# Kernel optimization log

Measured on AMD Instinct MI355X. Metric: run time of the kernel, lower is better.

## Reference

```python
import jax, jax.numpy as jnp
import numpy as np

B, S, V, H = 64, 512, 128, 1024
TEMP = 1.0


def _lstm_layer(x_seq, W_ih, W_hh, b_ih, b_hh):
    """x_seq: (S, B, D_in) -> (S, B, H). PyTorch gate order: i, f, g, o."""
    Hh = W_hh.shape[1]
    Bb = x_seq.shape[1]
    # precompute input projections for all timesteps: (S, B, 4H)
    xW = jnp.einsum('sbd,gd->sbg', x_seq, W_ih) + (b_ih + b_hh)

    def step(carry, xw_t):
        h, c = carry
        gates = xw_t + h @ W_hh.T  # (B, 4H)
        i, f, g, o = jnp.split(gates, 4, axis=-1)
        i = jax.nn.sigmoid(i)
        f = jax.nn.sigmoid(f)
        g = jnp.tanh(g)
        o = jax.nn.sigmoid(o)
        c = f * c + i * g
        h = o * jnp.tanh(c)
        return (h, c), h

    h0 = jnp.zeros((Bb, Hh), dtype=x_seq.dtype)
    c0 = jnp.zeros((Bb, Hh), dtype=x_seq.dtype)
    _, hs = jax.lax.scan(step, (h0, c0), xW)
    return hs  # (S, B, H)


def setup_inputs() -> dict:
    key = jax.random.key(0)
    ks = jax.random.split(key, 11)
    s = 1.0 / np.sqrt(H)
    u = lambda k, shape: jax.random.uniform(k, shape, jnp.float32, -s, s)
    return {
        'x': jax.random.normal(ks[0], (B, S, V), jnp.float32),
        'W_ih0': u(ks[1], (4 * H, V)),
        'W_hh0': u(ks[2], (4 * H, H)),
        'b_ih0': u(ks[3], (4 * H,)),
        'b_hh0': u(ks[4], (4 * H,)),
        'W_ih1': u(ks[5], (4 * H, H)),
        'W_hh1': u(ks[6], (4 * H, H)),
        'b_ih1': u(ks[7], (4 * H,)),
        'b_hh1': u(ks[8], (4 * H,)),
        'W_fc': u(ks[9], (V, H)),
        'b_fc': u(ks[10], (V,)),
    }


def reference(x, W_ih0, W_hh0, b_ih0, b_hh0, W_ih1, W_hh1, b_ih1, b_hh1, W_fc, b_fc):
    xs = jnp.transpose(x, (1, 0, 2))  # (S, B, V)
    h1 = _lstm_layer(xs, W_ih0, W_hh0, b_ih0, b_hh0)   # (S, B, H)
    h2 = _lstm_layer(h1, W_ih1, W_hh1, b_ih1, b_hh1)   # (S, B, H)
    logits = jnp.einsum('sbh,vh->sbv', h2, W_fc) + b_fc  # (S, B, V)
    out = jax.nn.log_softmax(logits * TEMP, axis=-1)
    return jnp.transpose(out, (1, 0, 2))  # (B, S, V)
```

## Files before the change

kernel.cpp:

```cpp
#include <hip/hip_runtime.h>
#include <hip/hip_bf16.h>
#include <math.h>


#define S_LEN 512
#define B_SZ  64
#define V_SZ  128
#define H_SZ  1024
#define BH    65536
#define RING  64
#define SLOT  66560
#define FSTR  16
#define INVP  48

typedef unsigned short u16;
typedef unsigned short u16x8 __attribute__((ext_vector_type(8)));
typedef __bf16         bf16x8 __attribute__((ext_vector_type(8)));
typedef float          f32x4  __attribute__((ext_vector_type(4)));
typedef int            i32x4  __attribute__((ext_vector_type(4)));

__device__ __forceinline__ u16 f2bf(float f) {
    unsigned int u = __float_as_uint(f);
    u += 0x7fffu + ((u >> 16) & 1u);
    return (u16)(u >> 16);
}
__device__ __forceinline__ f32x4 mfma16(u16x8 a, u16x8 b, f32x4 c) {
    return __builtin_amdgcn_mfma_f32_16x16x32_bf16(
        __builtin_bit_cast(bf16x8, a), __builtin_bit_cast(bf16x8, b), c, 0, 0, 0);
}
__device__ __forceinline__ f32x4 mfma16(i32x4 a, u16x8 b, f32x4 c) {
    return __builtin_amdgcn_mfma_f32_16x16x32_bf16(
        __builtin_bit_cast(bf16x8, a), __builtin_bit_cast(bf16x8, b), c, 0, 0, 0);
}

__device__ __forceinline__ void ld_g(i32x4& d, const u16* p) {
    asm volatile("global_load_dwordx4 %0, %1, off" : "=v"(d) : "v"(p));
}
__device__ __forceinline__ void st_coh_u16(u16* p, u16 v) {
    unsigned int vv = v;
    asm volatile("global_store_short %0, %1, off sc0 sc1" :: "v"(p), "v"(vv));
}
__device__ __forceinline__ int ld_flag(const int* p) {
    int v;
    asm volatile("global_load_dword %0, %1, off sc0 sc1\n\ts_waitcnt vmcnt(0)"
                 : "=v"(v) : "v"(p) : "memory");
    return v;
}
__device__ __forceinline__ void st_flag(int* p, int v) {
    asm volatile("global_store_dword %0, %1, off sc0 sc1" :: "v"(p), "v"(v));
}
#define WAITV(n) asm volatile("s_waitcnt vmcnt(" #n ")" ::: "memory")
#define SCHEDB   __builtin_amdgcn_sched_barrier(0)

__device__ __forceinline__ void l2_acquire_inv() {
    __builtin_amdgcn_fence(__ATOMIC_ACQUIRE, "agent");
}

__global__ __launch_bounds__(256) void cvt_kernel(const float* __restrict__ s,
                                                  u16* __restrict__ d, int n)
{
    int i = (blockIdx.x * 256 + threadIdx.x) * 4;
    if (i >= n) return;
    float4 v = *(const float4*)(s + i);
    ushort4 o;
    o.x = f2bf(v.x); o.y = f2bf(v.y); o.z = f2bf(v.z); o.w = f2bf(v.w);
    *(ushort4*)(d + i) = o;
}

union SMemL {
    struct { u16 wih[4 * 4 * 64 * 8]; u16 whh[32 * 4 * 64 * 8]; } l0;
    struct { u16 w[2 * 32 * 2 * 64 * 8]; } l1;
    float lg[16][132];
};

__global__ __launch_bounds__(256, 1) void persist_kernel(
    const float* __restrict__ x,
    const u16* __restrict__ Wih0c, const u16* __restrict__ Whh0c,
    const u16* __restrict__ Wih1c, const u16* __restrict__ Whh1c,
    const u16* __restrict__ Wfcc,
    const float* __restrict__ bih0, const float* __restrict__ bhh0,
    const float* __restrict__ bih1, const float* __restrict__ bhh1,
    const float* __restrict__ bfc,
    u16* __restrict__ h0b, u16* __restrict__ h1b,
    int* __restrict__ flagL0, int* __restrict__ flagL1, int* __restrict__ flagFC,
    float* __restrict__ out)
{
    __shared__ SMemL sm;
    const int bid = blockIdx.x, tid = threadIdx.x;
    const int wave = tid >> 6, lane = tid & 63;
    const int l16 = lane & 15, kgi = lane >> 4, kg8 = kgi * 8;

    if (bid < 64) {
        const int j0 = bid * 16, jj = j0 + l16;
        #pragma unroll
        for (int i = 0; i < 4; ++i) {
            int f = tid + i * 256;
            int rl = f >> 4, kf = f & 15;
            int c = kf >> 2, kg = kf & 3;
            int g = rl >> 4, jl = rl & 15;
            int gr = g * H_SZ + j0 + jl;
            *(u16x8*)&sm.l0.wih[(((c * 4 + g) * 64) + kg * 16 + jl) * 8] =
                *(const u16x8*)(Wih0c + (size_t)gr * V_SZ + kf * 8);
        }
        #pragma unroll
        for (int i = 0; i < 32; ++i) {
            int f = tid + i * 256;
            int rl = f >> 7, kf = f & 127;
            int c = kf >> 2, kg = kf & 3;
            int g = rl >> 4, jl = rl & 15;
            int gr = g * H_SZ + j0 + jl;
            *(u16x8*)&sm.l0.whh[(((c * 4 + g) * 64) + kg * 16 + jl) * 8] =
                *(const u16x8*)(Whh0c + (size_t)gr * H_SZ + kf * 8);
        }
        __syncthreads();

        const float bii = bih0[jj]            + bhh0[jj];
        const float bif = bih0[H_SZ + jj]     + bhh0[H_SZ + jj];
        const float big = bih0[2 * H_SZ + jj] + bhh0[2 * H_SZ + jj];
        const float bio = bih0[3 * H_SZ + jj] + bhh0[3 * H_SZ + jj];

        const int arow = wave * 16 + l16;
        const float* xrow = x + (size_t)arow * (S_LEN * V_SZ);
        float creg[4] = {0.f, 0.f, 0.f, 0.f};

        for (int t = 0; t < S_LEN; ++t) {
            {
                const int* p = nullptr; int tgt = 0;
                if (tid < 64)                        { p = flagL0 + tid * FSTR;        tgt = t; }
                else if (tid < 192 && t >= RING)     { p = flagL1 + (tid - 64) * FSTR; tgt = t - (RING - 1); }
                if (p && tgt > 0) while (ld_flag(p) < tgt) __builtin_amdgcn_s_sleep(2);
                __syncthreads();
            }
            if (t >= INVP && (t % INVP) == 0) l2_acquire_inv();

            f32x4 acc[4][2] = {};
            {
                const float* xp = xrow + (size_t)t * V_SZ + kg8;
                #pragma unroll
                for (int i = 0; i < 4; ++i) {
                    float4 u = *(const float4*)(xp + i * 32);
                    float4 v = *(const float4*)(xp + i * 32 + 4);
                    u16x8 af;
                    af[0] = f2bf(u.x); af[1] = f2bf(u.y); af[2] = f2bf(u.z); af[3] = f2bf(u.w);
                    af[4] = f2bf(v.x); af[5] = f2bf(v.y); af[6] = f2bf(v.z); af[7] = f2bf(v.w);
                    #pragma unroll
                    for (int g = 0; g < 4; ++g)
                        acc[g][i & 1] = mfma16(af,
                            *(const u16x8*)&sm.l0.wih[((i * 4 + g) * 64 + lane) * 8], acc[g][i & 1]);
                }
            }
            {
                auto ISSUE = [&](i32x4 (&buf)[8], const u16* base) {
                    #pragma unroll
                    for (int q = 0; q < 8; ++q) ld_g(buf[q], base + q * 32);
                };
                auto COMP = [&](i32x4 (&buf)[8], int k0) {
                    #pragma unroll
                    for (int q = 0; q < 8; ++q) {
                        #pragma unroll
                        for (int g = 0; g < 4; ++g)
                            acc[g][q & 1] = mfma16(buf[q],
                                *(const u16x8*)&sm.l0.whh[(((k0 + q) * 4 + g) * 64 + lane) * 8],
                                acc[g][q & 1]);
                    }
                };
                const u16* aB = h0b + (size_t)((t - 1) & (RING - 1)) * SLOT
                              + (size_t)arow * H_SZ + kg8;
                i32x4 b0[8], b1[8];
                WAITV(0);
                ISSUE(b0, aB);
                ISSUE(b1, aB + 256); WAITV(8); SCHEDB; COMP(b0, 0);
                ISSUE(b0, aB + 512); WAITV(8); SCHEDB; COMP(b1, 8);
                ISSUE(b1, aB + 768); WAITV(8); SCHEDB; COMP(b0, 16);
                                     WAITV(0); SCHEDB; COMP(b1, 24);
            }
            {
                u16* hout = h0b + (size_t)(t & (RING - 1)) * SLOT;
                #pragma unroll
                for (int r = 0; r < 4; ++r) {
                    const int m = wave * 16 + kgi * 4 + r;
                    const float ip = acc[0][0][r] + acc[0][1][r] + bii;
                    const float fp = acc[1][0][r] + acc[1][1][r] + bif;
                    const float gp = acc[2][0][r] + acc[2][1][r] + big;
                    const float op = acc[3][0][r] + acc[3][1][r] + bio;
                    const float iv = 1.f / (1.f + expf(-ip));
                    const float fv = 1.f / (1.f + expf(-fp));
                    const float gv = tanhf(gp);
                    const float ov = 1.f / (1.f + expf(-op));
                    const float cv = fv * creg[r] + iv * gv;
                    creg[r] = cv;
                    st_coh_u16(hout + (size_t)m * H_SZ + jj, f2bf(ov * tanhf(cv)));
                }
                WAITV(0);
            }
            __syncthreads();
            if (tid == 0) st_flag(flagL0 + bid * FSTR, t + 1);
        }
        return;
    }

    if (bid < 192) {
        const int lb = bid - 64, j0 = lb * 8, jj2 = j0 + (l16 & 7);
        #pragma unroll
        for (int i = 0; i < 32; ++i) {
            int f = tid + i * 256;
            int region = f >> 12;
            int r2 = f & 4095;
            int rl = r2 >> 7, kf = r2 & 127;
            int c = kf >> 2, kg = kf & 3;
            int nt = rl >> 4, jl = rl & 15;
            int gr = (rl >> 3) * H_SZ + j0 + (rl & 7);
            const u16* src = (region ? Whh1c : Wih1c) + (size_t)gr * H_SZ + kf * 8;
            *(u16x8*)&sm.l1.w[((((region * 32 + c) * 2 + nt) * 64) + kg * 16 + jl) * 8] =
                *(const u16x8*)src;
        }
        __syncthreads();

        const float bii = bih1[jj2]            + bhh1[jj2];
        const float bif = bih1[H_SZ + jj2]     + bhh1[H_SZ + jj2];
        const float big = bih1[2 * H_SZ + jj2] + bhh1[2 * H_SZ + jj2];
        const float bio = bih1[3 * H_SZ + jj2] + bhh1[3 * H_SZ + jj2];
        const bool lo = (l16 < 8);

        const int arow = wave * 16 + l16;
        float creg[4] = {0.f, 0.f, 0.f, 0.f};

        for (int t = 0; t < S_LEN; ++t) {
            {
                const int* p = nullptr; int tgt = 0;
                if (tid < 64)                        { p = flagL0 + tid * FSTR;         tgt = t + 1; }
                else if (tid < 192)                  { p = flagL1 + (tid - 64) * FSTR;  tgt = t; }
                else if (tid < 196 && t >= RING)     { p = flagFC + (tid - 192) * FSTR; tgt = t - (RING - 1); }
                if (p && tgt > 0) while (ld_flag(p) < tgt) __builtin_amdgcn_s_sleep(2);
                __syncthreads();
            }
            if (t >= INVP && (t % INVP) == 0) l2_acquire_inv();

            f32x4 acc[2][2] = {};
            {
                auto ISSUE = [&](i32x4 (&buf)[8], const u16* base) {
                    #pragma unroll
                    for (int q = 0; q < 8; ++q) ld_g(buf[q], base + q * 32);
                };
                auto COMP = [&](i32x4 (&buf)[8], int region, int c0) {
                    #pragma unroll
                    for (int q = 0; q < 8; ++q) {
                        #pragma unroll
                        for (int nt = 0; nt < 2; ++nt)
                            acc[nt][q & 1] = mfma16(buf[q],
                                *(const u16x8*)&sm.l1.w[(((region * 32 + c0 + q) * 2 + nt) * 64 + lane) * 8],
                                acc[nt][q & 1]);
                    }
                };
                const u16* a1 = h0b + (size_t)(t & (RING - 1)) * SLOT
                              + (size_t)arow * H_SZ + kg8;
                const u16* a2 = h1b + (size_t)((t - 1) & (RING - 1)) * SLOT
                              + (size_t)arow * H_SZ + kg8;
                i32x4 b0[8], b1[8];
                WAITV(0);
                ISSUE(b0, a1);
                ISSUE(b1, a1 + 256); WAITV(8); SCHEDB; COMP(b0, 0, 0);
                ISSUE(b0, a1 + 512); WAITV(8); SCHEDB; COMP(b1, 0, 8);
                ISSUE(b1, a1 + 768); WAITV(8); SCHEDB; COMP(b0, 0, 16);
                ISSUE(b0, a2);       WAITV(8); SCHEDB; COMP(b1, 0, 24);
                ISSUE(b1, a2 + 256); WAITV(8); SCHEDB; COMP(b0, 1, 0);
                ISSUE(b0, a2 + 512); WAITV(8); SCHEDB; COMP(b1, 1, 8);
                ISSUE(b1, a2 + 768); WAITV(8); SCHEDB; COMP(b0, 1, 16);
                                     WAITV(0); SCHEDB; COMP(b1, 1, 24);
            }
            {
                u16* hout = h1b + (size_t)(t & (RING - 1)) * SLOT;
                #pragma unroll
                for (int r = 0; r < 4; ++r) {
                    const float s0 = acc[0][0][r] + acc[0][1][r];
                    const float s1 = acc[1][0][r] + acc[1][1][r];
                    const float q0 = __shfl_xor(s0, 8);
                    const float q1 = __shfl_xor(s1, 8);
                    const float ip = (lo ? s0 : q0) + bii;
                    const float fp = (lo ? q0 : s0) + bif;
                    const float gp = (lo ? s1 : q1) + big;
                    const float op = (lo ? q1 : s1) + bio;
                    const float iv = 1.f / (1.f + expf(-ip));
                    const float fv = 1.f / (1.f + expf(-fp));
                    const float gv = tanhf(gp);
                    const float ov = 1.f / (1.f + expf(-op));
                    const float cv = fv * creg[r] + iv * gv;
                    creg[r] = cv;
                    if (lo) {
                        const int m = wave * 16 + kgi * 4 + r;
                        st_coh_u16(hout + (size_t)m * H_SZ + jj2, f2bf(ov * tanhf(cv)));
                    }
                }
                WAITV(0);
            }
            __syncthreads();
            if (tid == 0) st_flag(flagL1 + lb * FSTR, t + 1);
        }
        return;
    }

    {
        const int fb = bid - 192, m0 = fb * 16;
        const u16* wp[2];
        #pragma unroll
        for (int nt = 0; nt < 2; ++nt)
            wp[nt] = Wfcc + (size_t)(wave * 32 + nt * 16 + l16) * H_SZ + kg8;

        for (int t = 0; t < S_LEN; ++t) {
            {
                const int* p = nullptr; int tgt = 0;
                if (tid < 128) { p = flagL1 + tid * FSTR; tgt = t + 1; }
                if (p && tgt > 0) while (ld_flag(p) < tgt) __builtin_amdgcn_s_sleep(2);
                __syncthreads();
            }
            if (t >= INVP && (t % INVP) == 0) l2_acquire_inv();

            const u16* aB = h1b + (size_t)(t & (RING - 1)) * SLOT
                          + (size_t)(m0 + l16) * H_SZ + kg8;
            f32x4 acc[2][2] = {};
            i32x4 buf[8];
            WAITV(0);
            #pragma unroll
            for (int c = 0; c < 4; ++c) {
                #pragma unroll
                for (int q = 0; q < 8; ++q) ld_g(buf[q], aB + c * 256 + q * 32);
                WAITV(0); SCHEDB;
                #pragma unroll
                for (int q = 0; q < 8; ++q) {
                    #pragma unroll
                    for (int nt = 0; nt < 2; ++nt)
                        acc[nt][q & 1] = mfma16(buf[q],
                            *(const u16x8*)(wp[nt] + (c * 8 + q) * 32), acc[nt][q & 1]);
                }
            }
            #pragma unroll
            for (int nt = 0; nt < 2; ++nt)
                #pragma unroll
                for (int r = 0; r < 4; ++r) {
                    const int m = kgi * 4 + r, n = wave * 32 + nt * 16 + l16;
                    sm.lg[m][n] = acc[nt][0][r] + acc[nt][1][r] + bfc[n];
                }
            __syncthreads();
            const int row = tid >> 4, sub = tid & 15;
            float vals[8]; float mx = -1e30f;
            #pragma unroll
            for (int q = 0; q < 8; ++q) { vals[q] = sm.lg[row][sub * 8 + q]; mx = fmaxf(mx, vals[q]); }
            #pragma unroll
            for (int o = 1; o < 16; o <<= 1) mx = fmaxf(mx, __shfl_xor(mx, o));
            float se = 0.f;
            #pragma unroll
            for (int q = 0; q < 8; ++q) se += expf(vals[q] - mx);
            #pragma unroll
            for (int o = 1; o < 16; o <<= 1) se += __shfl_xor(se, o);
            const float ls = mx + logf(se);
            float* op = out + (size_t)(m0 + row) * (S_LEN * V_SZ) + (size_t)t * V_SZ + sub * 8;
            #pragma unroll
            for (int q = 0; q < 8; ++q) op[q] = vals[q] - ls;

            __syncthreads();
            if (tid == 0) st_flag(flagFC + fb * FSTR, t + 1);
        }
    }
}

extern "C" void kernel_launch(void* const* d_in, const int* in_sizes, int n_in,
                              void* d_out, int out_size, void* d_ws, size_t ws_size,
                              hipStream_t stream)
{
    const float* x    = (const float*)d_in[0];
    const float* Wih0 = (const float*)d_in[1];
    const float* Whh0 = (const float*)d_in[2];
    const float* bih0 = (const float*)d_in[3];
    const float* bhh0 = (const float*)d_in[4];
    const float* Wih1 = (const float*)d_in[5];
    const float* Whh1 = (const float*)d_in[6];
    const float* bih1 = (const float*)d_in[7];
    const float* bhh1 = (const float*)d_in[8];
    const float* Wfc  = (const float*)d_in[9];
    const float* bfc  = (const float*)d_in[10];
    float* out = (float*)d_out;

    u16* wih0 = (u16*)d_ws;
    u16* whh0 = wih0 + (size_t)4096 * 128;
    u16* wih1 = whh0 + (size_t)4096 * 1024;
    u16* whh1 = wih1 + (size_t)4096 * 1024;
    u16* wfc  = whh1 + (size_t)4096 * 1024;
    u16* h0b  = wfc  + (size_t)128 * 1024;
    u16* h1b  = h0b + (size_t)RING * SLOT;
    int* flags  = (int*)(h1b + (size_t)RING * SLOT);
    int* flagL0 = flags;
    int* flagL1 = flagL0 + 64 * FSTR;
    int* flagFC = flagL1 + 128 * FSTR;

    auto cvt = [&](const float* s, u16* d, int n) {
        cvt_kernel<<<(n / 4 + 255) / 256, 256, 0, stream>>>(s, d, n);
    };
    cvt(Wih0, wih0, 4096 * 128);
    cvt(Whh0, whh0, 4096 * 1024);
    cvt(Wih1, wih1, 4096 * 1024);
    cvt(Whh1, whh1, 4096 * 1024);
    cvt(Wfc,  wfc,  128 * 1024);
    hipMemsetAsync(h0b + (size_t)(RING - 1) * SLOT, 0, (size_t)BH * sizeof(u16), stream);
    hipMemsetAsync(h1b + (size_t)(RING - 1) * SLOT, 0, (size_t)BH * sizeof(u16), stream);
    hipMemsetAsync(flags, 0, (size_t)196 * FSTR * sizeof(int), stream);

    persist_kernel<<<196, 256, 0, stream>>>(
        x, wih0, whh0, wih1, whh1, wfc,
        bih0, bhh0, bih1, bhh1, bfc,
        h0b, h1b, flagL0, flagL1, flagFC, out);
}
```

Measured before the change: 6.553 ms.

## Swizzle LDS weights, pre-convert x, vectorize h stores, deepen load pipeline

Stores the recurrent and input weights in LDS as row-major with an XOR swizzle instead of the MFMA-fragment layout. Converts x to bf16 in a separate pre-kernel and prefetches it before the flag wait. Each step's h output is staged through a small LDS transpose buffer so it can be written with coherent 16-byte stores instead of scattered 2-byte stores. The global h loads move to a three-buffer pipeline, and the ring depth and L2 invalidate period shrink. The aims are fewer tiny coherent stores per step, more load latency hidden, and less conversion work on the critical path, at the cost of an extra LDS round trip, more registers, and a smaller ring slack between layers.

```diff
diff --git a/kernel.cpp b/kernel.cpp
--- a/kernel.cpp
+++ b/kernel.cpp
@@ -8,10 +8,10 @@
 #define V_SZ  128
 #define H_SZ  1024
 #define BH    65536
-#define RING  64
+#define RING  32
 #define SLOT  66560
 #define FSTR  16
-#define INVP  48
+#define INVP  20
 
 typedef unsigned short u16;
 typedef unsigned short u16x8 __attribute__((ext_vector_type(8)));
@@ -36,9 +36,9 @@
 __device__ __forceinline__ void ld_g(i32x4& d, const u16* p) {
     asm volatile("global_load_dwordx4 %0, %1, off" : "=v"(d) : "v"(p));
 }
-__device__ __forceinline__ void st_coh_u16(u16* p, u16 v) {
-    unsigned int vv = v;
-    asm volatile("global_store_short %0, %1, off sc0 sc1" :: "v"(p), "v"(vv));
+__device__ __forceinline__ void st_coh16(u16* p, u16x8 v) {
+    i32x4 vv = __builtin_bit_cast(i32x4, v);
+    asm volatile("global_store_dwordx4 %0, %1, off sc0 sc1" :: "v"(p), "v"(vv));
 }
 __device__ __forceinline__ int ld_flag(const int* p) {
     int v;
@@ -50,6 +50,7 @@
     asm volatile("global_store_dword %0, %1, off sc0 sc1" :: "v"(p), "v"(v));
 }
 #define WAITV(n) asm volatile("s_waitcnt vmcnt(" #n ")" ::: "memory")
+#define LGKM0    asm volatile("s_waitcnt lgkmcnt(0)" ::: "memory")
 #define SCHEDB   __builtin_amdgcn_sched_barrier(0)
 
 __device__ __forceinline__ void l2_acquire_inv() {
@@ -68,13 +69,13 @@
 }
 
 union SMemL {
-    struct { u16 wih[4 * 4 * 64 * 8]; u16 whh[32 * 4 * 64 * 8]; } l0;
-    struct { u16 w[2 * 32 * 2 * 64 * 8]; } l1;
+    struct { u16 whh[64 * 1024]; u16 wih[64 * 128]; u16 tr[4][384]; } l0;
+    struct { u16 w[64 * 1024]; u16 tr[4][384]; } l1;
     float lg[16][132];
 };
 
 __global__ __launch_bounds__(256, 1) void persist_kernel(
-    const float* __restrict__ x,
+    const u16* __restrict__ xb,
     const u16* __restrict__ Wih0c, const u16* __restrict__ Whh0c,
     const u16* __restrict__ Wih1c, const u16* __restrict__ Whh1c,
     const u16* __restrict__ Wfcc,
@@ -92,25 +93,17 @@
 
     if (bid < 64) {
         const int j0 = bid * 16, jj = j0 + l16;
-        #pragma unroll
-        for (int i = 0; i < 4; ++i) {
-            int f = tid + i * 256;
-            int rl = f >> 4, kf = f & 15;
-            int c = kf >> 2, kg = kf & 3;
-            int g = rl >> 4, jl = rl & 15;
-            int gr = g * H_SZ + j0 + jl;
-            *(u16x8*)&sm.l0.wih[(((c * 4 + g) * 64) + kg * 16 + jl) * 8] =
-                *(const u16x8*)(Wih0c + (size_t)gr * V_SZ + kf * 8);
-        }
-        #pragma unroll
-        for (int i = 0; i < 32; ++i) {
-            int f = tid + i * 256;
-            int rl = f >> 7, kf = f & 127;
-            int c = kf >> 2, kg = kf & 3;
-            int g = rl >> 4, jl = rl & 15;
-            int gr = g * H_SZ + j0 + jl;
-            *(u16x8*)&sm.l0.whh[(((c * 4 + g) * 64) + kg * 16 + jl) * 8] =
-                *(const u16x8*)(Whh0c + (size_t)gr * H_SZ + kf * 8);
+        for (int ch = tid; ch < 1024; ch += 256) {
+            int row = ch >> 4, kc = ch & 15;
+            int gr = (row >> 4) * H_SZ + j0 + (row & 15);
+            int bo = (row * 256 + kc * 16) ^ ((row & 7) << 4);
+            *(u16x8*)((char*)sm.l0.wih + bo) = *(const u16x8*)(Wih0c + (size_t)gr * V_SZ + kc * 8);
+        }
+        for (int ch = tid; ch < 8192; ch += 256) {
+            int row = ch >> 7, kc = ch & 127;
+            int gr = (row >> 4) * H_SZ + j0 + (row & 15);
+            int bo = (row * 2048 + kc * 16) ^ ((row & 7) << 4);
+            *(u16x8*)((char*)sm.l0.whh + bo) = *(const u16x8*)(Whh0c + (size_t)gr * H_SZ + kc * 8);
         }
         __syncthreads();
 
@@ -119,66 +112,70 @@
         const float big = bih0[2 * H_SZ + jj] + bhh0[2 * H_SZ + jj];
         const float bio = bih0[3 * H_SZ + jj] + bhh0[3 * H_SZ + jj];
 
+        const int swz = (l16 & 7) << 4;
+        int whh_rb[4], wih_rb[4];
+        #pragma unroll
+        for (int g = 0; g < 4; ++g) {
+            whh_rb[g] = (g * 16 + l16) * 2048 + kgi * 16;
+            wih_rb[g] = (g * 16 + l16) * 256 + kgi * 16;
+        }
         const int arow = wave * 16 + l16;
-        const float* xrow = x + (size_t)arow * (S_LEN * V_SZ);
+        const u16* xrow = xb + (size_t)arow * (S_LEN * V_SZ);
+        u16* trw = sm.l0.tr[wave];
         float creg[4] = {0.f, 0.f, 0.f, 0.f};
 
         for (int t = 0; t < S_LEN; ++t) {
+            i32x4 xq[4];
+            {
+                const u16* xp = xrow + (size_t)t * V_SZ + kg8;
+                #pragma unroll
+                for (int i = 0; i < 4; ++i) ld_g(xq[i], xp + i * 32);
+            }
             {
                 const int* p = nullptr; int tgt = 0;
-                if (tid < 64)                        { p = flagL0 + tid * FSTR;        tgt = t; }
-                else if (tid < 192 && t >= RING)     { p = flagL1 + (tid - 64) * FSTR; tgt = t - (RING - 1); }
+                if (tid < 64)                      { p = flagL0 + tid * FSTR;        tgt = t; }
+                else if (tid < 192 && t >= RING)   { p = flagL1 + (tid - 64) * FSTR; tgt = t - (RING - 1); }
                 if (p && tgt > 0) while (ld_flag(p) < tgt) __builtin_amdgcn_s_sleep(2);
                 __syncthreads();
             }
             if (t >= INVP && (t % INVP) == 0) l2_acquire_inv();
+            WAITV(0); SCHEDB;
 
             f32x4 acc[4][2] = {};
-            {
-                const float* xp = xrow + (size_t)t * V_SZ + kg8;
-                #pragma unroll
-                for (int i = 0; i < 4; ++i) {
-                    float4 u = *(const float4*)(xp + i * 32);
-                    float4 v = *(const float4*)(xp + i * 32 + 4);
-                    u16x8 af;
-                    af[0] = f2bf(u.x); af[1] = f2bf(u.y); af[2] = f2bf(u.z); af[3] = f2bf(u.w);
-                    af[4] = f2bf(v.x); af[5] = f2bf(v.y); af[6] = f2bf(v.z); af[7] = f2bf(v.w);
+            auto ISSUE = [&](i32x4 (&buf)[8], const u16* base) {
+                #pragma unroll
+                for (int q = 0; q < 8; ++q) ld_g(buf[q], base + q * 32);
+            };
+            auto COMP = [&](i32x4 (&buf)[8], int k0) {
+                #pragma unroll
+                for (int q = 0; q < 8; ++q)
                     #pragma unroll
                     for (int g = 0; g < 4; ++g)
-                        acc[g][i & 1] = mfma16(af,
-                            *(const u16x8*)&sm.l0.wih[((i * 4 + g) * 64 + lane) * 8], acc[g][i & 1]);
-                }
-            }
-            {
-                auto ISSUE = [&](i32x4 (&buf)[8], const u16* base) {
-                    #pragma unroll
-                    for (int q = 0; q < 8; ++q) ld_g(buf[q], base + q * 32);
-                };
-                auto COMP = [&](i32x4 (&buf)[8], int k0) {
-                    #pragma unroll
-                    for (int q = 0; q < 8; ++q) {
-                        #pragma unroll
-                        for (int g = 0; g < 4; ++g)
-                            acc[g][q & 1] = mfma16(buf[q],
-                                *(const u16x8*)&sm.l0.whh[(((k0 + q) * 4 + g) * 64 + lane) * 8],
-                                acc[g][q & 1]);
-                    }
-                };
-                const u16* aB = h0b + (size_t)((t - 1) & (RING - 1)) * SLOT
-                              + (size_t)arow * H_SZ + kg8;
-                i32x4 b0[8], b1[8];
-                WAITV(0);
-                ISSUE(b0, aB);
-                ISSUE(b1, aB + 256); WAITV(8); SCHEDB; COMP(b0, 0);
-                ISSUE(b0, aB + 512); WAITV(8); SCHEDB; COMP(b1, 8);
-                ISSUE(b1, aB + 768); WAITV(8); SCHEDB; COMP(b0, 16);
-                                     WAITV(0); SCHEDB; COMP(b1, 24);
-            }
+                        acc[g][q & 1] = mfma16(buf[q],
+                            *(const u16x8*)((char*)sm.l0.whh + ((whh_rb[g] + (k0 + q) * 64) ^ swz)),
+                            acc[g][q & 1]);
+            };
+            const u16* aB = h0b + (size_t)((t - 1) & (RING - 1)) * SLOT
+                          + (size_t)arow * H_SZ + kg8;
+            i32x4 b0[8], b1[8], b2[8];
+            ISSUE(b0, aB); ISSUE(b1, aB + 256); ISSUE(b2, aB + 512);
+            SCHEDB;
+            #pragma unroll
+            for (int i = 0; i < 4; ++i)
+                #pragma unroll
+                for (int g = 0; g < 4; ++g)
+                    acc[g][i & 1] = mfma16(xq[i],
+                        *(const u16x8*)((char*)sm.l0.wih + ((wih_rb[g] + i * 64) ^ swz)),
+                        acc[g][i & 1]);
+            WAITV(16); SCHEDB; COMP(b0, 0);  ISSUE(b0, aB + 768);
+            WAITV(16); SCHEDB; COMP(b1, 8);
+            WAITV(8);  SCHEDB; COMP(b2, 16);
+            WAITV(0);  SCHEDB; COMP(b0, 24);
+
             {
                 u16* hout = h0b + (size_t)(t & (RING - 1)) * SLOT;
                 #pragma unroll
                 for (int r = 0; r < 4; ++r) {
-                    const int m = wave * 16 + kgi * 4 + r;
                     const float ip = acc[0][0][r] + acc[0][1][r] + bii;
                     const float fp = acc[1][0][r] + acc[1][1][r] + bif;
                     const float gp = acc[2][0][r] + acc[2][1][r] + big;
@@ -189,7 +186,13 @@
                     const float ov = 1.f / (1.f + expf(-op));
                     const float cv = fv * creg[r] + iv * gv;
                     creg[r] = cv;
-                    st_coh_u16(hout + (size_t)m * H_SZ + jj, f2bf(ov * tanhf(cv)));
+                    trw[(kgi * 4 + r) * 24 + l16] = f2bf(ov * tanhf(cv));
+                }
+                LGKM0; SCHEDB;
+                if (lane < 32) {
+                    int m = lane >> 1, jb = lane & 1;
+                    u16x8 v = *(const u16x8*)&trw[m * 24 + jb * 8];
+                    st_coh16(hout + (size_t)(wave * 16 + m) * H_SZ + j0 + jb * 8, v);
                 }
                 WAITV(0);
             }
@@ -201,18 +204,13 @@
 
     if (bid < 192) {
         const int lb = bid - 64, j0 = lb * 8, jj2 = j0 + (l16 & 7);
-        #pragma unroll
-        for (int i = 0; i < 32; ++i) {
-            int f = tid + i * 256;
-            int region = f >> 12;
-            int r2 = f & 4095;
-            int rl = r2 >> 7, kf = r2 & 127;
-            int c = kf >> 2, kg = kf & 3;
-            int nt = rl >> 4, jl = rl & 15;
+        for (int ch = tid; ch < 8192; ch += 256) {
+            int ldsrow = ch >> 7, kc = ch & 127;
+            int region = ldsrow >> 5, rl = ldsrow & 31;
             int gr = (rl >> 3) * H_SZ + j0 + (rl & 7);
-            const u16* src = (region ? Whh1c : Wih1c) + (size_t)gr * H_SZ + kf * 8;
-            *(u16x8*)&sm.l1.w[((((region * 32 + c) * 2 + nt) * 64) + kg * 16 + jl) * 8] =
-                *(const u16x8*)src;
+            const u16* src = (region ? Whh1c : Wih1c) + (size_t)gr * H_SZ + kc * 8;
+            int bo = (ldsrow * 2048 + kc * 16) ^ ((ldsrow & 7) << 4);
+            *(u16x8*)((char*)sm.l1.w + bo) = *(const u16x8*)src;
         }
         __syncthreads();
 
@@ -222,7 +220,15 @@
         const float bio = bih1[3 * H_SZ + jj2] + bhh1[3 * H_SZ + jj2];
         const bool lo = (l16 < 8);
 
+        const int swz = (l16 & 7) << 4;
+        int wrb[2][2];
+        #pragma unroll
+        for (int region = 0; region < 2; ++region)
+            #pragma unroll
+            for (int nt = 0; nt < 2; ++nt)
+                wrb[region][nt] = (region * 32 + nt * 16 + l16) * 2048 + kgi * 16;
         const int arow = wave * 16 + l16;
+        u16* trw = sm.l1.tr[wave];
         float creg[4] = {0.f, 0.f, 0.f, 0.f};
 
         for (int t = 0; t < S_LEN; ++t) {
@@ -237,39 +243,34 @@
             if (t >= INVP && (t % INVP) == 0) l2_acquire_inv();
 
             f32x4 acc[2][2] = {};
-            {
-                auto ISSUE = [&](i32x4 (&buf)[8], const u16* base) {
+            auto ISSUE = [&](i32x4 (&buf)[8], const u16* base) {
+                #pragma unroll
+                for (int q = 0; q < 8; ++q) ld_g(buf[q], base + q * 32);
+            };
+            auto COMP = [&](i32x4 (&buf)[8], int region, int k0) {
+                #pragma unroll
+                for (int q = 0; q < 8; ++q)
                     #pragma unroll
-                    for (int q = 0; q < 8; ++q) ld_g(buf[q], base + q * 32);
-                };
-                auto COMP = [&](i32x4 (&buf)[8], int region, int c0) {
-                    #pragma unroll
-                    for (int q = 0; q < 8; ++q) {
-                        #pragma unroll
-                        for (int nt = 0; nt < 2; ++nt)
-                            acc[nt][q & 1] = mfma16(buf[q],
-                                *(const u16x8*)&sm.l1.w[(((region * 32 + c0 + q) * 2 + nt) * 64 + lane) * 8],
-                                acc[nt][q & 1]);
-                    }
-                };
-                const u16* a1 = h0b + (size_t)(t & (RING - 1)) * SLOT
-                              + (size_t)arow * H_SZ + kg8;
-                const u16* a2 = h1b + (size_t)((t - 1) & (RING - 1)) * SLOT
-                              + (size_t)arow * H_SZ + kg8;
-                i32x4 b0[8], b1[8];
-                WAITV(0);
-                ISSUE(b0, a1);
-                ISSUE(b1, a1 + 256); WAITV(8); SCHEDB; COMP(b0, 0, 0);
-                ISSUE(b0, a1 + 512); WAITV(8); SCHEDB; COMP(b1, 0, 8);
-                ISSUE(b1, a1 + 768); WAITV(8); SCHEDB; COMP(b0, 0, 16);
-                ISSUE(b0, a2);       WAITV(8); SCHEDB; COMP(b1, 0, 24);
-                ISSUE(b1, a2 + 256); WAITV(8); SCHEDB; COMP(b0, 1, 0);
-                ISSUE(b0, a2 + 512); WAITV(8); SCHEDB; COMP(b1, 1, 8);
-                ISSUE(b1, a2 + 768); WAITV(8); SCHEDB; COMP(b0, 1, 16);
-                                     WAITV(0); SCHEDB; COMP(b1, 1, 24);
-            }
-            {
-                u16* hout = h1b + (size_t)(t & (RING - 1)) * SLOT;
+                    for (int nt = 0; nt < 2; ++nt)
+                        acc[nt][q & 1] = mfma16(buf[q],
+                            *(const u16x8*)((char*)sm.l1.w + ((wrb[region][nt] + (k0 + q) * 64) ^ swz)),
+                            acc[nt][q & 1]);
+            };
+            const u16* a1 = h0b + (size_t)(t & (RING - 1)) * SLOT + (size_t)arow * H_SZ + kg8;
+            const u16* a2 = h1b + (size_t)((t - 1) & (RING - 1)) * SLOT + (size_t)arow * H_SZ + kg8;
+            i32x4 b0[8], b1[8], b2[8];
+            ISSUE(b0, a1); ISSUE(b1, a1 + 256); ISSUE(b2, a1 + 512);
+            SCHEDB;
+            WAITV(16); SCHEDB; COMP(b0, 0, 0);  ISSUE(b0, a1 + 768);
+            WAITV(16); SCHEDB; COMP(b1, 0, 8);  ISSUE(b1, a2);
+            WAITV(16); SCHEDB; COMP(b2, 0, 16); ISSUE(b2, a2 + 256);
+            WAITV(16); SCHEDB; COMP(b0, 0, 24); ISSUE(b0, a2 + 512);
+            WAITV(16); SCHEDB; COMP(b1, 1, 0);  ISSUE(b1, a2 + 768);
+            WAITV(16); SCHEDB; COMP(b2, 1, 8);
+            WAITV(8);  SCHEDB; COMP(b0, 1, 16);
+            WAITV(0);  SCHEDB; COMP(b1, 1, 24);
+
+            {
                 #pragma unroll
                 for (int r = 0; r < 4; ++r) {
                     const float s0 = acc[0][0][r] + acc[0][1][r];
@@ -286,10 +287,14 @@
                     const float ov = 1.f / (1.f + expf(-op));
                     const float cv = fv * creg[r] + iv * gv;
                     creg[r] = cv;
-                    if (lo) {
-                        const int m = wave * 16 + kgi * 4 + r;
-                        st_coh_u16(hout + (size_t)m * H_SZ + jj2, f2bf(ov * tanhf(cv)));
-                    }
+                    if (lo) trw[(kgi * 4 + r) * 24 + (l16 & 7)] = f2bf(ov * tanhf(cv));
+                }
+                LGKM0; SCHEDB;
+                if (lane < 16) {
+                    int m = lane;
+                    u16x8 v = *(const u16x8*)&trw[m * 24];
+                    st_coh16(h1b + (size_t)(t & (RING - 1)) * SLOT
+                             + (size_t)(wave * 16 + m) * H_SZ + j0, v);
                 }
                 WAITV(0);
             }
@@ -385,7 +390,8 @@
     u16* wih1 = whh0 + (size_t)4096 * 1024;
     u16* whh1 = wih1 + (size_t)4096 * 1024;
     u16* wfc  = whh1 + (size_t)4096 * 1024;
-    u16* h0b  = wfc  + (size_t)128 * 1024;
+    u16* xbuf = wfc  + (size_t)128 * 1024;
+    u16* h0b  = xbuf + (size_t)B_SZ * S_LEN * V_SZ;
     u16* h1b  = h0b + (size_t)RING * SLOT;
     int* flags  = (int*)(h1b + (size_t)RING * SLOT);
     int* flagL0 = flags;
@@ -400,12 +406,13 @@
     cvt(Wih1, wih1, 4096 * 1024);
     cvt(Whh1, whh1, 4096 * 1024);
     cvt(Wfc,  wfc,  128 * 1024);
+    cvt(x,    xbuf, B_SZ * S_LEN * V_SZ);
     hipMemsetAsync(h0b + (size_t)(RING - 1) * SLOT, 0, (size_t)BH * sizeof(u16), stream);
     hipMemsetAsync(h1b + (size_t)(RING - 1) * SLOT, 0, (size_t)BH * sizeof(u16), stream);
     hipMemsetAsync(flags, 0, (size_t)196 * FSTR * sizeof(int), stream);
 
     persist_kernel<<<196, 256, 0, stream>>>(
-        x, wih0, whh0, wih1, whh1, wfc,
+        xbuf, wih0, whh0, wih1, whh1, wfc,
         bih0, bhh0, bih1, bhh1, bfc,
         h0b, h1b, flagL0, flagL1, flagFC, out);
 }
```

After: 6.385 ms. -2.6%, faster.
